# Kernel tuning notes

Hardware: AMD Instinct MI355X
Metric: run time of the kernel (lower is better)

## Reference

```python
import jax, jax.numpy as jnp
from jax import lax
import numpy as np

CHUNK = 64


def short_conv(x, w):
    # depthwise causal conv1d: x (B,L,D), w (D,K)
    L = x.shape[1]
    K = w.shape[1]
    xp = jnp.pad(x, ((0, 0), (K - 1, 0), (0, 0)))
    return sum(xp[:, j:j + L, :] * w[:, j] for j in range(K))


def o2b_weighted_delta_rule(k, q, v, b):
    # k,q,v,b: (B,L,H,D) float32, zero initial state
    B, L, H, D = k.shape
    C = CHUNK
    Nc = L // C

    def to_chunks(t):  # (B,L,H,D) -> (Nc,B,H,C,D)
        return t.transpose(0, 2, 1, 3).reshape(B, H, Nc, C, D).transpose(2, 0, 1, 3, 4)

    Kc, Qc, Vc, Bc = map(to_chunks, (k, q, v, b))
    eyeC = jnp.eye(C, dtype=jnp.float32)
    W0 = jnp.zeros((B, H, D, D), jnp.float32)
    Cf = float(C)

    def step(carry, xs):
        W_t, W_avg = carry
        i, Ki, Qi, Vi, Bi = xs
        KiT = jnp.swapaxes(Ki, -1, -2)
        T = jnp.tril(Bi @ KiT, k=-1)                      # (B,H,C,C) strictly lower
        inv = jnp.linalg.inv(eyeC + T)
        Ui = inv @ (Vi - Bi @ W_t)                        # (B,H,C,D)
        W_new = W_t + KiT @ Ui
        ts = (i * C).astype(jnp.float32)                  # init t == 0 for all batches
        idx = jnp.arange(1, C + 1, dtype=jnp.float32) + ts  # (C,)
        cs = jnp.cumsum(idx)
        weighted_idx = idx + idx.sum() - cs
        w_i = (weighted_idx / ((1 + ts + Cf) * (ts + Cf) / 2))[:, None]  # (C,1)
        coef1 = ts / (ts + Cf) * ((1 + ts) / (1 + ts + Cf))
        coef2 = Cf / (ts + Cf) * ((ts * 2 + 1 + Cf) / (1 + ts + Cf))
        W_avg_new = coef1 * W_avg + coef2 * W_t + KiT @ (Ui * w_i)
        tri0 = (1 + ts) * ts / 2
        a = (tri0 / (tri0 + cs))[:, None]                 # (C,1)
        c = 1.0 - a
        r = cs[:, None]                                   # (C,1)
        j_idx = (cs - idx)[None, :]                       # (1,C)
        T_mat = jnp.where(r >= j_idx, (r - j_idx) / (tri0 + r), 0.0)  # (C,C)
        O_i = (Qi @ W_avg) * a + (Qi @ W_t) * c + (T_mat * (Qi @ KiT)) @ Ui
        return (W_new, W_avg_new), O_i

    (_, _), O = lax.scan(step, (W0, W0), (jnp.arange(Nc), Kc, Qc, Vc, Bc))
    # O: (Nc,B,H,C,D) -> (B,L,H,D)
    return O.transpose(1, 2, 0, 3, 4).reshape(B, H, L, D).transpose(0, 2, 1, 3)


def setup_inputs() -> dict:
    key = jax.random.key(0)
    ks = jax.random.split(key, 9)
    B, L, Dm, H = 4, 2048, 1024, 16
    Dh, K = Dm // H, 4
    s = 0.02
    return {
        'x': jax.random.normal(ks[0], (B, L, Dm), jnp.float32),
        'Wk': s * jax.random.normal(ks[1], (Dm, Dm), jnp.float32),
        'bk': jnp.zeros((Dm,), jnp.float32),
        'Wq': s * jax.random.normal(ks[2], (Dm, Dm), jnp.float32),
        'bq': jnp.zeros((Dm,), jnp.float32),
        'Wv': s * jax.random.normal(ks[3], (Dm, Dm), jnp.float32),
        'bv': jnp.zeros((Dm,), jnp.float32),
        'Wbeta': s * jax.random.normal(ks[4], (H, Dm), jnp.float32),
        'bbeta': jnp.zeros((H,), jnp.float32),
        'conv_k': 0.1 * jax.random.normal(ks[5], (Dm, K), jnp.float32),
        'conv_q': 0.1 * jax.random.normal(ks[6], (Dm, K), jnp.float32),
        'conv_v': 0.1 * jax.random.normal(ks[7], (Dm, K), jnp.float32),
        'rms_w': jnp.ones((Dh,), jnp.float32),
        'Wout': s * jax.random.normal(ks[8], (Dm, Dm), jnp.float32),
        'bout': jnp.zeros((Dm,), jnp.float32),
    }


def reference(x, Wk, bk, Wq, bq, Wv, bv, Wbeta, bbeta, conv_k, conv_q, conv_v, rms_w, Wout, bout):
    B, L, Dm = x.shape
    H = Wbeta.shape[0]
    Dh = Dm // H
    k = short_conv(x @ Wk.T + bk, conv_k)
    q = short_conv(x @ Wq.T + bq, conv_q)
    v = short_conv(x @ Wv.T + bv, conv_v)
    beta = jax.nn.sigmoid(x @ Wbeta.T + bbeta)            # (B,L,H)
    k = k.reshape(B, L, H, Dh)
    q = q.reshape(B, L, H, Dh)
    v = jax.nn.silu(v.reshape(B, L, H, Dh))
    knorm = jnp.linalg.norm(k, axis=-1, keepdims=True)
    qnorm = jnp.linalg.norm(q, axis=-1, keepdims=True)
    k = k / (knorm + 1e-6)
    q = q / (qnorm + 1e-6)
    eta = beta  # eta coefficient = 1.0, ogd_mode='deltanet'
    b = eta[..., None] * k
    v = eta[..., None] * v
    o = o2b_weighted_delta_rule(k, q, v, b)               # (B,L,H,Dh)
    o = o * jax.lax.rsqrt(jnp.mean(o * o, axis=-1, keepdims=True) + 1e-6) * rms_w
    o = o.reshape(B, L, Dm)
    return o @ Wout.T + bout
```

## Files before the change

### kernel.cpp

```cpp
#include <hip/hip_runtime.h>

typedef __attribute__((ext_vector_type(8))) short bf16x8;
typedef __attribute__((ext_vector_type(4))) float f32x4;

#define MFMA(a, b, c) __builtin_amdgcn_mfma_f32_16x16x32_bf16((a), (b), (c), 0, 0, 0)

__device__ inline unsigned short f2bf_rne(float f) {
  unsigned int u = __float_as_uint(f);
  u += 0x7FFFu + ((u >> 16) & 1u);
  return (unsigned short)(u >> 16);
}

__global__ __launch_bounds__(256) void cast_bf16_kernel(const float* __restrict__ in,
                                                        unsigned short* __restrict__ out,
                                                        int n4) {
  const int i = blockIdx.x * 256 + threadIdx.x;
  if (i >= n4) return;
  const float4 v = ((const float4*)in)[i];
  ushort4 o;
  o.x = f2bf_rne(v.x); o.y = f2bf_rne(v.y); o.z = f2bf_rne(v.z); o.w = f2bf_rne(v.w);
  ((ushort4*)out)[i] = o;
}

__global__ __launch_bounds__(256) void concat_bias_kernel(const float* __restrict__ bk,
                                                          const float* __restrict__ bq,
                                                          const float* __restrict__ bv,
                                                          float* __restrict__ b3) {
  const int i = blockIdx.x * 256 + threadIdx.x;
  if (i < 1024) b3[i] = bk[i];
  else if (i < 2048) b3[i] = bq[i - 1024];
  else if (i < 3072) b3[i] = bv[i - 2048];
}

__global__ __launch_bounds__(256) void gemm_bf16_nt(
    const unsigned short* __restrict__ A, const unsigned short* __restrict__ Bw,
    const float* __restrict__ bias, float* __restrict__ C, int M, int N, int K) {
  __shared__ unsigned short Asl[128 * 32];
  __shared__ unsigned short Bsl[128 * 32];
  const int tid = threadIdx.x;
  const int lane = tid & 63, w = tid >> 6;
  const int bm = blockIdx.x * 128, bn = blockIdx.y * 128;
  const int wr = (w >> 1) * 64, wc = (w & 1) * 64;

  const int li0 = tid, li1 = tid + 256;
  const int ar0 = li0 >> 2, ak0 = (li0 & 3) * 8;
  const int ar1 = li1 >> 2, ak1 = (li1 & 3) * 8;
  const unsigned short* gA0 = A + (size_t)(bm + ar0) * K + ak0;
  const unsigned short* gA1 = A + (size_t)(bm + ar1) * K + ak1;
  const unsigned short* gB0 = Bw + (size_t)(bn + ar0) * K + ak0;
  const unsigned short* gB1 = Bw + (size_t)(bn + ar1) * K + ak1;
  unsigned short* lA0 = &Asl[(size_t)(w * 64) * 8];
  unsigned short* lA1 = &Asl[(size_t)(w * 64 + 256) * 8];
  unsigned short* lB0 = &Bsl[(size_t)(w * 64) * 8];
  unsigned short* lB1 = &Bsl[(size_t)(w * 64 + 256) * 8];

  f32x4 acc[4][4];
#pragma unroll
  for (int i = 0; i < 4; ++i)
#pragma unroll
    for (int j = 0; j < 4; ++j) acc[i][j] = (f32x4){0.f, 0.f, 0.f, 0.f};

  const int fr = lane & 15, kg = lane >> 4;

  for (int k0 = 0; k0 < K; k0 += 32) {
    __syncthreads();
    __builtin_amdgcn_global_load_lds((const __attribute__((address_space(1))) unsigned int*)(gA0 + k0),
                                     (__attribute__((address_space(3))) unsigned int*)lA0, 16, 0, 0);
    __builtin_amdgcn_global_load_lds((const __attribute__((address_space(1))) unsigned int*)(gA1 + k0),
                                     (__attribute__((address_space(3))) unsigned int*)lA1, 16, 0, 0);
    __builtin_amdgcn_global_load_lds((const __attribute__((address_space(1))) unsigned int*)(gB0 + k0),
                                     (__attribute__((address_space(3))) unsigned int*)lB0, 16, 0, 0);
    __builtin_amdgcn_global_load_lds((const __attribute__((address_space(1))) unsigned int*)(gB1 + k0),
                                     (__attribute__((address_space(3))) unsigned int*)lB1, 16, 0, 0);
    __syncthreads();

    bf16x8 af[4], bfr[4];
#pragma unroll
    for (int i = 0; i < 4; ++i) {
      af[i] = *(const bf16x8*)&Asl[(size_t)(wr + i * 16 + fr) * 32 + kg * 8];
      bfr[i] = *(const bf16x8*)&Bsl[(size_t)(wc + i * 16 + fr) * 32 + kg * 8];
    }
#pragma unroll
    for (int i = 0; i < 4; ++i)
#pragma unroll
      for (int j = 0; j < 4; ++j)
        acc[i][j] = MFMA(af[i], bfr[j], acc[i][j]);
  }

  const int og = lane >> 4;
#pragma unroll
  for (int j = 0; j < 4; ++j) {
    const int col = bn + wc + j * 16 + fr;
    const float bs = bias[col];
#pragma unroll
    for (int i = 0; i < 4; ++i) {
#pragma unroll
      for (int r = 0; r < 4; ++r) {
        const int row = bm + wr + i * 16 + og * 4 + r;
        C[(size_t)row * N + col] = acc[i][j][r] + bs;
      }
    }
  }
}

__global__ __launch_bounds__(256) void beta_kernel(const float* __restrict__ x,
                                                   const float* __restrict__ Wb,
                                                   const float* __restrict__ bb,
                                                   float* __restrict__ beta) {
  const int m = blockIdx.x;
  const int tid = threadIdx.x;
  const int h = tid >> 4;
  const int l = tid & 15;
  const float4* x4 = (const float4*)(x + (size_t)m * 1024);
  const float4* w4 = (const float4*)(Wb + (size_t)h * 1024);
  float acc = 0.f;
#pragma unroll 4
  for (int jj = 0; jj < 16; ++jj) {
    float4 xv = x4[l + 16 * jj];
    float4 wv = w4[l + 16 * jj];
    acc += xv.x * wv.x + xv.y * wv.y + xv.z * wv.z + xv.w * wv.w;
  }
  acc += __shfl_xor(acc, 1);
  acc += __shfl_xor(acc, 2);
  acc += __shfl_xor(acc, 4);
  acc += __shfl_xor(acc, 8);
  if (l == 0) {
    const float s = acc + bb[h];
    beta[(size_t)m * 16 + h] = 1.f / (1.f + expf(-s));
  }
}

__global__ __launch_bounds__(256) void prep_kernel(
    const float* __restrict__ qkv, const float* __restrict__ betab,
    const float* __restrict__ convk, const float* __restrict__ convq,
    const float* __restrict__ convv,
    unsigned short* __restrict__ kn16, unsigned short* __restrict__ qn16,
    float* __restrict__ vz) {
  const int m = blockIdx.x;
  const int l = m & 2047;
  const int lane = threadIdx.x & 63;
  const int wvi = threadIdx.x >> 6;
#pragma unroll
  for (int s = 0; s < 4; ++s) {
    const int h = 4 * s + wvi;
    const int c = h * 64 + lane;
    const float4 wk4 = *(const float4*)(convk + (size_t)c * 4);
    const float4 wq4 = *(const float4*)(convq + (size_t)c * 4);
    const float4 wv4 = *(const float4*)(convv + (size_t)c * 4);
    const float wk[4] = {wk4.x, wk4.y, wk4.z, wk4.w};
    const float wq[4] = {wq4.x, wq4.y, wq4.z, wq4.w};
    const float wvv[4] = {wv4.x, wv4.y, wv4.z, wv4.w};
    float kc = 0.f, qc = 0.f, vc = 0.f;
#pragma unroll
    for (int j = 0; j < 4; ++j) {
      const int lj = l - 3 + j;
      if (lj >= 0) {
        const size_t rb = (size_t)(m - l + lj) * 3072 + c;
        kc += wk[j] * qkv[rb];
        qc += wq[j] * qkv[rb + 1024];
        vc += wvv[j] * qkv[rb + 2048];
      }
    }
    float ssk = kc * kc, ssq = qc * qc;
    ssk += __shfl_xor(ssk, 1); ssq += __shfl_xor(ssq, 1);
    ssk += __shfl_xor(ssk, 2); ssq += __shfl_xor(ssq, 2);
    ssk += __shfl_xor(ssk, 4); ssq += __shfl_xor(ssq, 4);
    ssk += __shfl_xor(ssk, 8); ssq += __shfl_xor(ssq, 8);
    ssk += __shfl_xor(ssk, 16); ssq += __shfl_xor(ssq, 16);
    ssk += __shfl_xor(ssk, 32); ssq += __shfl_xor(ssq, 32);
    const float eta = betab[(size_t)m * 16 + h];
    const size_t o = (size_t)m * 1024 + c;
    kn16[o] = f2bf_rne(kc / (sqrtf(ssk) + 1e-6f));
    qn16[o] = f2bf_rne(qc / (sqrtf(ssq) + 1e-6f));
    vz[o] = eta * vc / (1.f + expf(-vc));
  }
}

#define LDB 72
#define LDV 68

__global__ __launch_bounds__(512, 1) void scan_kernel(
    const unsigned short* __restrict__ kn16, const unsigned short* __restrict__ qn16,
    const float* __restrict__ vz, const float* __restrict__ betab,
    float* __restrict__ O) {
  __shared__ unsigned short Kb[64 * LDB], Qb[64 * LDB], Ktb[64 * LDB];
  __shared__ unsigned short Wtb[64 * LDB], Wavgtb[64 * LDB];
  __shared__ unsigned short Pb[2][64 * LDB], Ptb[2][64 * LDB], Ztb[2][64 * LDB];
  __shared__ unsigned short P1b[64 * LDB], Utwb[64 * LDB];
  __shared__ float Vs[64 * LDV];
  __shared__ float etas[64];

  const int tid = threadIdx.x;
  const int bh = blockIdx.x;
  const int b = bh >> 4, h = bh & 15;
  const int wv = tid >> 6, lane = tid & 63;
  const int fr = lane & 15, og = lane >> 4;
  const int i0 = (wv >> 2) * 2, i1 = i0 + 1, j = wv & 3;
  const int gcol = j * 16 + fr;
  const int row0 = i0 * 16 + og * 4;
  const int row1 = i1 * 16 + og * 4;

  for (int t = tid; t < 64 * LDB; t += 512) { Wtb[t] = 0; Wavgtb[t] = 0; }

  const size_t base = ((size_t)b * 2048) * 1024 + (size_t)h * 64;
  const unsigned short* kp = kn16 + base;
  const unsigned short* qp = qn16 + base;
  const float* vp = vz + base;
  const float* etap = betab + (size_t)b * 2048 * 16 + h;
  float* Op = O + (size_t)bh * 2048 * 64;

  f32x4 Wt[2], Wav[2];
  Wt[0] = Wt[1] = Wav[0] = Wav[1] = (f32x4){0.f, 0.f, 0.f, 0.f};

  const int sr = tid >> 3, sc8 = (tid & 7) * 8;
  __syncthreads();

#pragma unroll 1
  for (int ic = 0; ic < 32; ++ic) {
    const float ts = (float)(ic * 64);

    {
      const size_t g = (size_t)(ic * 64 + sr) * 1024 + sc8;
      *(ushort4*)&Kb[sr * LDB + sc8] = *(const ushort4*)(kp + g);
      *(ushort4*)&Kb[sr * LDB + sc8 + 4] = *(const ushort4*)(kp + g + 4);
      *(ushort4*)&Qb[sr * LDB + sc8] = *(const ushort4*)(qp + g);
      *(ushort4*)&Qb[sr * LDB + sc8 + 4] = *(const ushort4*)(qp + g + 4);
      *(float4*)&Vs[sr * LDV + sc8] = *(const float4*)(vp + g);
      *(float4*)&Vs[sr * LDV + sc8 + 4] = *(const float4*)(vp + g + 4);
      unsigned short tv[8];
#pragma unroll
      for (int i = 0; i < 8; ++i)
        tv[i] = kp[(size_t)(ic * 64 + sc8 + i) * 1024 + sr];
      ushort4 t0v = {tv[0], tv[1], tv[2], tv[3]}, t1v = {tv[4], tv[5], tv[6], tv[7]};
      *(ushort4*)&Ktb[sr * LDB + sc8] = t0v;
      *(ushort4*)&Ktb[sr * LDB + sc8 + 4] = t1v;
      if (tid < 64) etas[tid] = etap[(size_t)(ic * 64 + tid) * 16];
    }
    __syncthreads();

    f32x4 Zacc[2], RHSs[2];
    {
      bf16x8 aK0[2], aK1[2], bK[2], bW[2];
#pragma unroll
      for (int t = 0; t < 2; ++t) {
        aK0[t] = *(const bf16x8*)&Kb[(i0 * 16 + fr) * LDB + t * 32 + og * 8];
        aK1[t] = *(const bf16x8*)&Kb[(i1 * 16 + fr) * LDB + t * 32 + og * 8];
        bK[t] = *(const bf16x8*)&Kb[(j * 16 + fr) * LDB + t * 32 + og * 8];
        bW[t] = *(const bf16x8*)&Wtb[(j * 16 + fr) * LDB + t * 32 + og * 8];
      }
      f32x4 accT0 = {0, 0, 0, 0}, accT1 = {0, 0, 0, 0};
      f32x4 accR0 = {0, 0, 0, 0}, accR1 = {0, 0, 0, 0};
#pragma unroll
      for (int t = 0; t < 2; ++t) {
        accT0 = MFMA(aK0[t], bK[t], accT0);
        accT1 = MFMA(aK1[t], bK[t], accT1);
        accR0 = MFMA(aK0[t], bW[t], accR0);
        accR1 = MFMA(aK1[t], bW[t], accR1);
      }
#pragma unroll
      for (int s = 0; s < 2; ++s) {
        const int rb = s ? row1 : row0;
        const f32x4 aT = s ? accT1 : accT0;
        const f32x4 aR = s ? accR1 : accR0;
        unsigned short us[4];
        float zv[4];
#pragma unroll
        for (int r = 0; r < 4; ++r) {
          const int grow = rb + r;
          const float eta = etas[grow];
          const float tvv = (gcol < grow) ? -eta * aT[r] : 0.f;
          us[r] = f2bf_rne(tvv);
          zv[r] = Vs[grow * LDV + gcol] - eta * aR[r];
          Pb[0][grow * LDB + gcol] = us[r];
          P1b[grow * LDB + gcol] = us[r];
        }
        ushort4 pp = {us[0], us[1], us[2], us[3]};
        *(ushort4*)&Ptb[0][gcol * LDB + rb] = pp;
        ushort4 zp = {f2bf_rne(zv[0]), f2bf_rne(zv[1]), f2bf_rne(zv[2]), f2bf_rne(zv[3])};
        *(ushort4*)&Ztb[0][gcol * LDB + rb] = zp;
        Zacc[s] = (f32x4){zv[0], zv[1], zv[2], zv[3]};
        RHSs[s] = Zacc[s];
      }
    }
    __syncthreads();

#pragma unroll
    for (int k = 0; k < 6; ++k) {
      const int cur = k & 1, nxt = cur ^ 1;
      bf16x8 aP0[2], aP1[2], bZ[2];
#pragma unroll
      for (int t = 0; t < 2; ++t) {
        aP0[t] = *(const bf16x8*)&Pb[cur][(i0 * 16 + fr) * LDB + t * 32 + og * 8];
        aP1[t] = *(const bf16x8*)&Pb[cur][(i1 * 16 + fr) * LDB + t * 32 + og * 8];
        bZ[t] = *(const bf16x8*)&Ztb[cur][(j * 16 + fr) * LDB + t * 32 + og * 8];
      }
      f32x4 sq0 = {0, 0, 0, 0}, sq1 = {0, 0, 0, 0};
      if (k < 5) {
#pragma unroll
        for (int t = 0; t < 2; ++t) {
          bf16x8 bPt = *(const bf16x8*)&Ptb[cur][(j * 16 + fr) * LDB + t * 32 + og * 8];
          sq0 = MFMA(aP0[t], bPt, sq0);
          sq1 = MFMA(aP1[t], bPt, sq1);
        }
      }
#pragma unroll
      for (int t = 0; t < 2; ++t) {
        Zacc[0] = MFMA(aP0[t], bZ[t], Zacc[0]);
        Zacc[1] = MFMA(aP1[t], bZ[t], Zacc[1]);
      }
#pragma unroll
      for (int s = 0; s < 2; ++s) {
        const int rb = s ? row1 : row0;
        const f32x4 zz = Zacc[s];
        ushort4 zp = {f2bf_rne(zz[0]), f2bf_rne(zz[1]), f2bf_rne(zz[2]), f2bf_rne(zz[3])};
        *(ushort4*)&Ztb[nxt][gcol * LDB + rb] = zp;
        if (k < 5) {
          const f32x4 sv = s ? sq1 : sq0;
          unsigned short u0 = f2bf_rne(sv[0]), u1 = f2bf_rne(sv[1]);
          unsigned short u2 = f2bf_rne(sv[2]), u3 = f2bf_rne(sv[3]);
          Pb[nxt][(rb + 0) * LDB + gcol] = u0;
          Pb[nxt][(rb + 1) * LDB + gcol] = u1;
          Pb[nxt][(rb + 2) * LDB + gcol] = u2;
          Pb[nxt][(rb + 3) * LDB + gcol] = u3;
          ushort4 pp = {u0, u1, u2, u3};
          *(ushort4*)&Ptb[nxt][gcol * LDB + rb] = pp;
        }
      }
      __syncthreads();
    }

    bf16x8 a0[2], a1[2];
    {
#pragma unroll
      for (int t = 0; t < 2; ++t) {
        a0[t] = *(const bf16x8*)&P1b[(i0 * 16 + fr) * LDB + t * 32 + og * 8];
        a1[t] = *(const bf16x8*)&P1b[(i1 * 16 + fr) * LDB + t * 32 + og * 8];
      }
      f32x4 R0 = RHSs[0] - Zacc[0];
      f32x4 R1 = RHSs[1] - Zacc[1];
#pragma unroll
      for (int t = 0; t < 2; ++t) {
        bf16x8 bU = *(const bf16x8*)&Ztb[0][(j * 16 + fr) * LDB + t * 32 + og * 8];
        R0 = MFMA(a0[t], bU, R0);
        R1 = MFMA(a1[t], bU, R1);
      }
      ushort4 r0p = {f2bf_rne(R0[0]), f2bf_rne(R0[1]), f2bf_rne(R0[2]), f2bf_rne(R0[3])};
      ushort4 r1p = {f2bf_rne(R1[0]), f2bf_rne(R1[1]), f2bf_rne(R1[2]), f2bf_rne(R1[3])};
      *(ushort4*)&Pb[1][gcol * LDB + row0] = r0p;
      *(ushort4*)&Pb[1][gcol * LDB + row1] = r1p;
      RHSs[0] = R0;
      RHSs[1] = R1;
    }
    __syncthreads();

    {
      f32x4 dU0 = RHSs[0], dU1 = RHSs[1];
#pragma unroll
      for (int t = 0; t < 2; ++t) {
        bf16x8 bR = *(const bf16x8*)&Pb[1][(j * 16 + fr) * LDB + t * 32 + og * 8];
        dU0 = MFMA(a0[t], bR, dU0);
        dU1 = MFMA(a1[t], bR, dU1);
      }
      Zacc[0] += dU0;
      Zacc[1] += dU1;
      const float invden = 1.f / (0.5f * (ts + 65.f) * (ts + 64.f));
#pragma unroll
      for (int s = 0; s < 2; ++s) {
        const int rb = s ? row1 : row0;
        const f32x4 uu = Zacc[s];
        ushort4 up = {f2bf_rne(uu[0]), f2bf_rne(uu[1]), f2bf_rne(uu[2]), f2bf_rne(uu[3])};
        *(ushort4*)&Ztb[0][gcol * LDB + rb] = up;
        unsigned short uw[4];
#pragma unroll
        for (int r = 0; r < 4; ++r) {
          const float rr = (float)(rb + r);
          const float wr = (ts * (64.f - rr) + (rr + 1.f) + 2080.f -
                            0.5f * (rr + 1.f) * (rr + 2.f)) * invden;
          uw[r] = f2bf_rne(uu[r] * wr);
        }
        ushort4 uwp = {uw[0], uw[1], uw[2], uw[3]};
        *(ushort4*)&Utwb[gcol * LDB + rb] = uwp;
      }
    }
    f32x4 Oacc[2];
    {
      bf16x8 aQ0[2], aQ1[2], bKj[2], bWt2[2], bWa2[2];
#pragma unroll
      for (int t = 0; t < 2; ++t) {
        aQ0[t] = *(const bf16x8*)&Qb[(i0 * 16 + fr) * LDB + t * 32 + og * 8];
        aQ1[t] = *(const bf16x8*)&Qb[(i1 * 16 + fr) * LDB + t * 32 + og * 8];
        bKj[t] = *(const bf16x8*)&Kb[(j * 16 + fr) * LDB + t * 32 + og * 8];
        bWt2[t] = *(const bf16x8*)&Wtb[(j * 16 + fr) * LDB + t * 32 + og * 8];
        bWa2[t] = *(const bf16x8*)&Wavgtb[(j * 16 + fr) * LDB + t * 32 + og * 8];
      }
      f32x4 aS0 = {0, 0, 0, 0}, aS1 = {0, 0, 0, 0};
      f32x4 aA0 = {0, 0, 0, 0}, aA1 = {0, 0, 0, 0};
      f32x4 aC0 = {0, 0, 0, 0}, aC1 = {0, 0, 0, 0};
#pragma unroll
      for (int t = 0; t < 2; ++t) {
        aS0 = MFMA(aQ0[t], bKj[t], aS0);
        aS1 = MFMA(aQ1[t], bKj[t], aS1);
        aA0 = MFMA(aQ0[t], bWa2[t], aA0);
        aA1 = MFMA(aQ1[t], bWa2[t], aA1);
        aC0 = MFMA(aQ0[t], bWt2[t], aC0);
        aC1 = MFMA(aQ1[t], bWt2[t], aC1);
      }
      const float tri0 = 0.5f * ts * (ts + 1.f);
      const float jidx = gcol * ts + 0.5f * gcol * (gcol + 1.f);
#pragma unroll
      for (int s = 0; s < 2; ++s) {
        const int rb = s ? row1 : row0;
        const f32x4 sS = s ? aS1 : aS0;
        const f32x4 sA = s ? aA1 : aA0;
        const f32x4 sC = s ? aC1 : aC0;
        f32x4 oo;
#pragma unroll
        for (int r = 0; r < 4; ++r) {
          const float grow = (float)(rb + r);
          const float csr = (grow + 1.f) * ts + 0.5f * (grow + 1.f) * (grow + 2.f);
          const float rinv = 1.f / (tri0 + csr);
          const float av = tri0 * rinv;
          oo[r] = av * sA[r] + (1.f - av) * sC[r];
          const float svv = (csr >= jidx) ? (csr - jidx) * rinv * sS[r] : 0.f;
          Ptb[1][(rb + r) * LDB + gcol] = f2bf_rne(svv);
        }
        Oacc[s] = oo;
      }
    }
    __syncthreads();

    {
      bf16x8 aS0[2], aS1[2], bU2[2];
#pragma unroll
      for (int t = 0; t < 2; ++t) {
        aS0[t] = *(const bf16x8*)&Ptb[1][(i0 * 16 + fr) * LDB + t * 32 + og * 8];
        aS1[t] = *(const bf16x8*)&Ptb[1][(i1 * 16 + fr) * LDB + t * 32 + og * 8];
        bU2[t] = *(const bf16x8*)&Ztb[0][(j * 16 + fr) * LDB + t * 32 + og * 8];
      }
#pragma unroll
      for (int t = 0; t < 2; ++t) {
        Oacc[0] = MFMA(aS0[t], bU2[t], Oacc[0]);
        Oacc[1] = MFMA(aS1[t], bU2[t], Oacc[1]);
      }
#pragma unroll
      for (int s = 0; s < 2; ++s) {
        const int rb = s ? row1 : row0;
#pragma unroll
        for (int r = 0; r < 4; ++r)
          Op[(size_t)(ic * 64 + rb + r) * 64 + gcol] = Oacc[s][r];
      }
    }

    {
      bf16x8 aU0[2], aU1[2], aW0[2], aW1[2], bKt2[2];
#pragma unroll
      for (int t = 0; t < 2; ++t) {
        aU0[t] = *(const bf16x8*)&Ztb[0][(i0 * 16 + fr) * LDB + t * 32 + og * 8];
        aU1[t] = *(const bf16x8*)&Ztb[0][(i1 * 16 + fr) * LDB + t * 32 + og * 8];
        aW0[t] = *(const bf16x8*)&Utwb[(i0 * 16 + fr) * LDB + t * 32 + og * 8];
        aW1[t] = *(const bf16x8*)&Utwb[(i1 * 16 + fr) * LDB + t * 32 + og * 8];
        bKt2[t] = *(const bf16x8*)&Ktb[(j * 16 + fr) * LDB + t * 32 + og * 8];
      }
      const float den = (ts + 64.f) * (ts + 65.f);
      const float cc1 = ts * (ts + 1.f) / den;
      const float cc2 = 64.f * (2.f * ts + 65.f) / den;
      f32x4 wn0 = cc1 * Wav[0] + cc2 * Wt[0];
      f32x4 wn1 = cc1 * Wav[1] + cc2 * Wt[1];
#pragma unroll
      for (int t = 0; t < 2; ++t) {
        wn0 = MFMA(aW0[t], bKt2[t], wn0);
        wn1 = MFMA(aW1[t], bKt2[t], wn1);
        Wt[0] = MFMA(aU0[t], bKt2[t], Wt[0]);
        Wt[1] = MFMA(aU1[t], bKt2[t], Wt[1]);
      }
      Wav[0] = wn0;
      Wav[1] = wn1;
#pragma unroll
      for (int s = 0; s < 2; ++s) {
        const int rb = s ? row1 : row0;
        const f32x4 wtv = Wt[s];
        const f32x4 wav2 = Wav[s];
#pragma unroll
        for (int r = 0; r < 4; ++r) {
          Wtb[(rb + r) * LDB + gcol] = f2bf_rne(wtv[r]);
          Wavgtb[(rb + r) * LDB + gcol] = f2bf_rne(wav2[r]);
        }
      }
    }
    __syncthreads();
  }
}

__global__ __launch_bounds__(256) void rms_kernel(const float* __restrict__ O,
                                                  const float* __restrict__ rmsw,
                                                  unsigned short* __restrict__ out16) {
  const int m = blockIdx.x;
  const int b = m >> 11, l = m & 2047;
  const int wv = threadIdx.x >> 6, lane = threadIdx.x & 63;
  const float rw = rmsw[lane];
#pragma unroll
  for (int hh = 0; hh < 4; ++hh) {
    const int h = wv * 4 + hh;
    const float v = O[(((size_t)(b * 16 + h)) * 2048 + l) * 64 + lane];
    float ss = v * v;
    ss += __shfl_xor(ss, 1); ss += __shfl_xor(ss, 2); ss += __shfl_xor(ss, 4);
    ss += __shfl_xor(ss, 8); ss += __shfl_xor(ss, 16); ss += __shfl_xor(ss, 32);
    const float sc = rsqrtf(ss * (1.f / 64.f) + 1e-6f);
    out16[(size_t)m * 1024 + h * 64 + lane] = f2bf_rne(v * sc * rw);
  }
}

extern "C" void kernel_launch(void* const* d_in, const int* in_sizes, int n_in,
                              void* d_out, int out_size, void* d_ws, size_t ws_size,
                              hipStream_t stream) {
  (void)in_sizes; (void)n_in; (void)out_size; (void)ws_size;
  const float* x     = (const float*)d_in[0];
  const float* Wk    = (const float*)d_in[1];
  const float* bk    = (const float*)d_in[2];
  const float* Wq    = (const float*)d_in[3];
  const float* bq    = (const float*)d_in[4];
  const float* Wv    = (const float*)d_in[5];
  const float* bv    = (const float*)d_in[6];
  const float* Wbeta = (const float*)d_in[7];
  const float* bbeta = (const float*)d_in[8];
  const float* convk = (const float*)d_in[9];
  const float* convq = (const float*)d_in[10];
  const float* convv = (const float*)d_in[11];
  const float* rmsw  = (const float*)d_in[12];
  const float* Wout  = (const float*)d_in[13];
  const float* bout  = (const float*)d_in[14];
  float* out = (float*)d_out;
  float* ws = (float*)d_ws;

  const size_t SZ = (size_t)8192 * 1024;
  float* qkv = ws;
  float* betab = ws + 3 * SZ;
  unsigned short* x16 = (unsigned short*)(ws + 3 * SZ + 131072);
  unsigned short* wk16 = x16 + SZ;
  unsigned short* wq16 = wk16 + 1048576;
  unsigned short* wv16 = wq16 + 1048576;
  unsigned short* wo16 = wv16 + 1048576;
  unsigned short* kn16 = wo16 + 1048576;
  unsigned short* qn16 = kn16 + SZ;
  float* b3 = (float*)(qn16 + SZ);
  float* vzb = out;
  float* Obuf = qkv;
  unsigned short* normed16 = (unsigned short*)(ws + SZ);

  dim3 blk(256);
  hipLaunchKernelGGL(cast_bf16_kernel, dim3(8192), blk, 0, stream, x, x16, (int)(SZ / 4));
  hipLaunchKernelGGL(cast_bf16_kernel, dim3(1024), blk, 0, stream, Wk, wk16, 262144);
  hipLaunchKernelGGL(cast_bf16_kernel, dim3(1024), blk, 0, stream, Wq, wq16, 262144);
  hipLaunchKernelGGL(cast_bf16_kernel, dim3(1024), blk, 0, stream, Wv, wv16, 262144);
  hipLaunchKernelGGL(cast_bf16_kernel, dim3(1024), blk, 0, stream, Wout, wo16, 262144);
  hipLaunchKernelGGL(concat_bias_kernel, dim3(12), blk, 0, stream, bk, bq, bv, b3);

  hipLaunchKernelGGL(gemm_bf16_nt, dim3(64, 24), blk, 0, stream, x16, wk16, b3,
                     qkv, 8192, 3072, 1024);
  hipLaunchKernelGGL(beta_kernel, dim3(8192), blk, 0, stream, x, Wbeta, bbeta, betab);
  hipLaunchKernelGGL(prep_kernel, dim3(8192), blk, 0, stream, qkv, betab,
                     convk, convq, convv, kn16, qn16, vzb);
  hipLaunchKernelGGL(scan_kernel, dim3(64), dim3(512), 0, stream, kn16, qn16, vzb,
                     betab, Obuf);
  hipLaunchKernelGGL(rms_kernel, dim3(8192), blk, 0, stream, Obuf, rmsw, normed16);
  hipLaunchKernelGGL(gemm_bf16_nt, dim3(64, 8), blk, 0, stream, normed16, wo16, bout, out,
                     8192, 1024, 1024);
}
```

Measured before the change: 586.1 us.

## Prefetch next chunk in scan, fuse cast and beta kernels into fewer launches

The scan kernel now double-buffers K and Q in shared memory and prefetches the next chunk's K, Q, transposed K, V and eta into registers while the current chunk computes. This removes the per-chunk load phase and its barrier from the serial critical path. Separately, the five cast kernels and the bias concat are merged into one grid-stride kernel, and the beta projection plus sigmoid is folded into prep_kernel, cutting launches and a global round trip. The cost is higher register and shared-memory use in the scan kernel, plus redundant final-chunk loads.

```diff
diff --git a/kernel.cpp b/kernel.cpp
--- a/kernel.cpp
+++ b/kernel.cpp
@@ -11,25 +11,37 @@
   return (unsigned short)(u >> 16);
 }
 
-__global__ __launch_bounds__(256) void cast_bf16_kernel(const float* __restrict__ in,
-                                                        unsigned short* __restrict__ out,
-                                                        int n4) {
-  const int i = blockIdx.x * 256 + threadIdx.x;
-  if (i >= n4) return;
-  const float4 v = ((const float4*)in)[i];
-  ushort4 o;
-  o.x = f2bf_rne(v.x); o.y = f2bf_rne(v.y); o.z = f2bf_rne(v.z); o.w = f2bf_rne(v.w);
-  ((ushort4*)out)[i] = o;
-}
-
-__global__ __launch_bounds__(256) void concat_bias_kernel(const float* __restrict__ bk,
-                                                          const float* __restrict__ bq,
-                                                          const float* __restrict__ bv,
-                                                          float* __restrict__ b3) {
-  const int i = blockIdx.x * 256 + threadIdx.x;
-  if (i < 1024) b3[i] = bk[i];
-  else if (i < 2048) b3[i] = bq[i - 1024];
-  else if (i < 3072) b3[i] = bv[i - 2048];
+__global__ __launch_bounds__(256) void prepare_kernel(
+    const float* __restrict__ x, const float* __restrict__ Wk,
+    const float* __restrict__ Wq, const float* __restrict__ Wv,
+    const float* __restrict__ Wout, const float* __restrict__ bk,
+    const float* __restrict__ bq, const float* __restrict__ bv,
+    unsigned short* __restrict__ x16, unsigned short* __restrict__ wk16,
+    unsigned short* __restrict__ wq16, unsigned short* __restrict__ wv16,
+    unsigned short* __restrict__ wo16, float* __restrict__ b3) {
+  const int gid = blockIdx.x * 256 + threadIdx.x;
+  const int stride = gridDim.x * 256;
+  for (int i = gid; i < 2097152; i += stride) {
+    const float4 v = ((const float4*)x)[i];
+    ushort4 o = {f2bf_rne(v.x), f2bf_rne(v.y), f2bf_rne(v.z), f2bf_rne(v.w)};
+    ((ushort4*)x16)[i] = o;
+  }
+  for (int i = gid; i < 262144; i += stride) {
+    float4 v = ((const float4*)Wk)[i];
+    ushort4 o = {f2bf_rne(v.x), f2bf_rne(v.y), f2bf_rne(v.z), f2bf_rne(v.w)};
+    ((ushort4*)wk16)[i] = o;
+    v = ((const float4*)Wq)[i];
+    o = (ushort4){f2bf_rne(v.x), f2bf_rne(v.y), f2bf_rne(v.z), f2bf_rne(v.w)};
+    ((ushort4*)wq16)[i] = o;
+    v = ((const float4*)Wv)[i];
+    o = (ushort4){f2bf_rne(v.x), f2bf_rne(v.y), f2bf_rne(v.z), f2bf_rne(v.w)};
+    ((ushort4*)wv16)[i] = o;
+    v = ((const float4*)Wout)[i];
+    o = (ushort4){f2bf_rne(v.x), f2bf_rne(v.y), f2bf_rne(v.z), f2bf_rne(v.w)};
+    ((ushort4*)wo16)[i] = o;
+  }
+  if (gid < 3072)
+    b3[gid] = gid < 1024 ? bk[gid] : gid < 2048 ? bq[gid - 1024] : bv[gid - 2048];
 }
 
 __global__ __launch_bounds__(256) void gemm_bf16_nt(
@@ -103,43 +115,45 @@
   }
 }
 
-__global__ __launch_bounds__(256) void beta_kernel(const float* __restrict__ x,
-                                                   const float* __restrict__ Wb,
-                                                   const float* __restrict__ bb,
-                                                   float* __restrict__ beta) {
-  const int m = blockIdx.x;
-  const int tid = threadIdx.x;
-  const int h = tid >> 4;
-  const int l = tid & 15;
-  const float4* x4 = (const float4*)(x + (size_t)m * 1024);
-  const float4* w4 = (const float4*)(Wb + (size_t)h * 1024);
-  float acc = 0.f;
-#pragma unroll 4
-  for (int jj = 0; jj < 16; ++jj) {
-    float4 xv = x4[l + 16 * jj];
-    float4 wv = w4[l + 16 * jj];
-    acc += xv.x * wv.x + xv.y * wv.y + xv.z * wv.z + xv.w * wv.w;
-  }
-  acc += __shfl_xor(acc, 1);
-  acc += __shfl_xor(acc, 2);
-  acc += __shfl_xor(acc, 4);
-  acc += __shfl_xor(acc, 8);
-  if (l == 0) {
-    const float s = acc + bb[h];
-    beta[(size_t)m * 16 + h] = 1.f / (1.f + expf(-s));
-  }
-}
-
 __global__ __launch_bounds__(256) void prep_kernel(
-    const float* __restrict__ qkv, const float* __restrict__ betab,
+    const float* __restrict__ x, const float* __restrict__ qkv,
+    const float* __restrict__ Wbeta, const float* __restrict__ bbeta,
     const float* __restrict__ convk, const float* __restrict__ convq,
-    const float* __restrict__ convv,
+    const float* __restrict__ convv, float* __restrict__ betab,
     unsigned short* __restrict__ kn16, unsigned short* __restrict__ qn16,
     float* __restrict__ vz) {
+  __shared__ float etas_sm[16];
   const int m = blockIdx.x;
   const int l = m & 2047;
   const int lane = threadIdx.x & 63;
   const int wvi = threadIdx.x >> 6;
+
+  {
+    const float4* xr = (const float4*)(x + (size_t)m * 1024);
+    const float4 xv0 = xr[lane], xv1 = xr[lane + 64];
+    const float4 xv2 = xr[lane + 128], xv3 = xr[lane + 192];
+#pragma unroll
+    for (int hh = 0; hh < 4; ++hh) {
+      const int h = wvi * 4 + hh;
+      const float4* wr = (const float4*)(Wbeta + (size_t)h * 1024);
+      const float4 w0 = wr[lane], w1 = wr[lane + 64];
+      const float4 w2 = wr[lane + 128], w3 = wr[lane + 192];
+      float acc = xv0.x * w0.x + xv0.y * w0.y + xv0.z * w0.z + xv0.w * w0.w +
+                  xv1.x * w1.x + xv1.y * w1.y + xv1.z * w1.z + xv1.w * w1.w +
+                  xv2.x * w2.x + xv2.y * w2.y + xv2.z * w2.z + xv2.w * w2.w +
+                  xv3.x * w3.x + xv3.y * w3.y + xv3.z * w3.z + xv3.w * w3.w;
+      acc += __shfl_xor(acc, 1); acc += __shfl_xor(acc, 2);
+      acc += __shfl_xor(acc, 4); acc += __shfl_xor(acc, 8);
+      acc += __shfl_xor(acc, 16); acc += __shfl_xor(acc, 32);
+      if (lane == 0) {
+        const float e = 1.f / (1.f + expf(-(acc + bbeta[h])));
+        etas_sm[h] = e;
+        betab[(size_t)m * 16 + h] = e;
+      }
+    }
+  }
+  __syncthreads();
+
 #pragma unroll
   for (int s = 0; s < 4; ++s) {
     const int h = 4 * s + wvi;
@@ -152,13 +166,13 @@
     const float wvv[4] = {wv4.x, wv4.y, wv4.z, wv4.w};
     float kc = 0.f, qc = 0.f, vc = 0.f;
 #pragma unroll
-    for (int j = 0; j < 4; ++j) {
-      const int lj = l - 3 + j;
+    for (int jj = 0; jj < 4; ++jj) {
+      const int lj = l - 3 + jj;
       if (lj >= 0) {
         const size_t rb = (size_t)(m - l + lj) * 3072 + c;
-        kc += wk[j] * qkv[rb];
-        qc += wq[j] * qkv[rb + 1024];
-        vc += wvv[j] * qkv[rb + 2048];
+        kc += wk[jj] * qkv[rb];
+        qc += wq[jj] * qkv[rb + 1024];
+        vc += wvv[jj] * qkv[rb + 2048];
       }
     }
     float ssk = kc * kc, ssq = qc * qc;
@@ -168,7 +182,7 @@
     ssk += __shfl_xor(ssk, 8); ssq += __shfl_xor(ssq, 8);
     ssk += __shfl_xor(ssk, 16); ssq += __shfl_xor(ssq, 16);
     ssk += __shfl_xor(ssk, 32); ssq += __shfl_xor(ssq, 32);
-    const float eta = betab[(size_t)m * 16 + h];
+    const float eta = etas_sm[h];
     const size_t o = (size_t)m * 1024 + c;
     kn16[o] = f2bf_rne(kc / (sqrtf(ssk) + 1e-6f));
     qn16[o] = f2bf_rne(qc / (sqrtf(ssq) + 1e-6f));
@@ -177,18 +191,15 @@
 }
 
 #define LDB 72
-#define LDV 68
 
 __global__ __launch_bounds__(512, 1) void scan_kernel(
     const unsigned short* __restrict__ kn16, const unsigned short* __restrict__ qn16,
     const float* __restrict__ vz, const float* __restrict__ betab,
     float* __restrict__ O) {
-  __shared__ unsigned short Kb[64 * LDB], Qb[64 * LDB], Ktb[64 * LDB];
+  __shared__ unsigned short Kb[2][64 * LDB], Qb[2][64 * LDB], Ktb[64 * LDB];
   __shared__ unsigned short Wtb[64 * LDB], Wavgtb[64 * LDB];
   __shared__ unsigned short Pb[2][64 * LDB], Ptb[2][64 * LDB], Ztb[2][64 * LDB];
   __shared__ unsigned short P1b[64 * LDB], Utwb[64 * LDB];
-  __shared__ float Vs[64 * LDV];
-  __shared__ float etas[64];
 
   const int tid = threadIdx.x;
   const int bh = blockIdx.x;
@@ -213,39 +224,66 @@
   Wt[0] = Wt[1] = Wav[0] = Wav[1] = (f32x4){0.f, 0.f, 0.f, 0.f};
 
   const int sr = tid >> 3, sc8 = (tid & 7) * 8;
+
+  {
+    const size_t g = (size_t)sr * 1024 + sc8;
+    *(ushort4*)&Kb[0][sr * LDB + sc8] = *(const ushort4*)(kp + g);
+    *(ushort4*)&Kb[0][sr * LDB + sc8 + 4] = *(const ushort4*)(kp + g + 4);
+    *(ushort4*)&Qb[0][sr * LDB + sc8] = *(const ushort4*)(qp + g);
+    *(ushort4*)&Qb[0][sr * LDB + sc8 + 4] = *(const ushort4*)(qp + g + 4);
+    ushort4 t0v, t1v;
+    t0v.x = kp[(size_t)(sc8 + 0) * 1024 + sr];
+    t0v.y = kp[(size_t)(sc8 + 1) * 1024 + sr];
+    t0v.z = kp[(size_t)(sc8 + 2) * 1024 + sr];
+    t0v.w = kp[(size_t)(sc8 + 3) * 1024 + sr];
+    t1v.x = kp[(size_t)(sc8 + 4) * 1024 + sr];
+    t1v.y = kp[(size_t)(sc8 + 5) * 1024 + sr];
+    t1v.z = kp[(size_t)(sc8 + 6) * 1024 + sr];
+    t1v.w = kp[(size_t)(sc8 + 7) * 1024 + sr];
+    *(ushort4*)&Ktb[sr * LDB + sc8] = t0v;
+    *(ushort4*)&Ktb[sr * LDB + sc8 + 4] = t1v;
+  }
+  float vr0[4], vr1[4], er0[4], er1[4];
+#pragma unroll
+  for (int r = 0; r < 4; ++r) {
+    vr0[r] = vp[(size_t)(row0 + r) * 1024 + gcol];
+    vr1[r] = vp[(size_t)(row1 + r) * 1024 + gcol];
+    er0[r] = etap[(size_t)(row0 + r) * 16];
+    er1[r] = etap[(size_t)(row1 + r) * 16];
+  }
+  ushort4 pk0, pk1, pq0, pq1, pt0, pt1;
   __syncthreads();
 
 #pragma unroll 1
   for (int ic = 0; ic < 32; ++ic) {
+    const int cur = ic & 1, nxt = cur ^ 1;
     const float ts = (float)(ic * 64);
-
-    {
-      const size_t g = (size_t)(ic * 64 + sr) * 1024 + sc8;
-      *(ushort4*)&Kb[sr * LDB + sc8] = *(const ushort4*)(kp + g);
-      *(ushort4*)&Kb[sr * LDB + sc8 + 4] = *(const ushort4*)(kp + g + 4);
-      *(ushort4*)&Qb[sr * LDB + sc8] = *(const ushort4*)(qp + g);
-      *(ushort4*)&Qb[sr * LDB + sc8 + 4] = *(const ushort4*)(qp + g + 4);
-      *(float4*)&Vs[sr * LDV + sc8] = *(const float4*)(vp + g);
-      *(float4*)&Vs[sr * LDV + sc8 + 4] = *(const float4*)(vp + g + 4);
-      unsigned short tv[8];
-#pragma unroll
-      for (int i = 0; i < 8; ++i)
-        tv[i] = kp[(size_t)(ic * 64 + sc8 + i) * 1024 + sr];
-      ushort4 t0v = {tv[0], tv[1], tv[2], tv[3]}, t1v = {tv[4], tv[5], tv[6], tv[7]};
-      *(ushort4*)&Ktb[sr * LDB + sc8] = t0v;
-      *(ushort4*)&Ktb[sr * LDB + sc8 + 4] = t1v;
-      if (tid < 64) etas[tid] = etap[(size_t)(ic * 64 + tid) * 16];
-    }
-    __syncthreads();
+    const int icn = (ic < 31) ? ic + 1 : ic;
 
     f32x4 Zacc[2], RHSs[2];
     {
+      if (ic > 0) {
+        *(ushort4*)&Ktb[sr * LDB + sc8] = pt0;
+        *(ushort4*)&Ktb[sr * LDB + sc8 + 4] = pt1;
+      }
+      const size_t gn = (size_t)(icn * 64 + sr) * 1024 + sc8;
+      pk0 = *(const ushort4*)(kp + gn);
+      pk1 = *(const ushort4*)(kp + gn + 4);
+      pq0 = *(const ushort4*)(qp + gn);
+      pq1 = *(const ushort4*)(qp + gn + 4);
+      {
+        const size_t cb = (size_t)(icn * 64 + sc8);
+        pt0.x = kp[(cb + 0) * 1024 + sr]; pt0.y = kp[(cb + 1) * 1024 + sr];
+        pt0.z = kp[(cb + 2) * 1024 + sr]; pt0.w = kp[(cb + 3) * 1024 + sr];
+        pt1.x = kp[(cb + 4) * 1024 + sr]; pt1.y = kp[(cb + 5) * 1024 + sr];
+        pt1.z = kp[(cb + 6) * 1024 + sr]; pt1.w = kp[(cb + 7) * 1024 + sr];
+      }
       bf16x8 aK0[2], aK1[2], bK[2], bW[2];
 #pragma unroll
       for (int t = 0; t < 2; ++t) {
-        aK0[t] = *(const bf16x8*)&Kb[(i0 * 16 + fr) * LDB + t * 32 + og * 8];
-        aK1[t] = *(const bf16x8*)&Kb[(i1 * 16 + fr) * LDB + t * 32 + og * 8];
-        bK[t] = *(const bf16x8*)&Kb[(j * 16 + fr) * LDB + t * 32 + og * 8];
+        aK0[t] = *(const bf16x8*)&Kb[cur][(i0 * 16 + fr) * LDB + t * 32 + og * 8];
+        aK1[t] = *(const bf16x8*)&Kb[cur][(i1 * 16 + fr) * LDB + t * 32 + og * 8];
+        bK[t] = *(const bf16x8*)&Kb[cur][(j * 16 + fr) * LDB + t * 32 + og * 8];
         bW[t] = *(const bf16x8*)&Wtb[(j * 16 + fr) * LDB + t * 32 + og * 8];
       }
       f32x4 accT0 = {0, 0, 0, 0}, accT1 = {0, 0, 0, 0};
@@ -267,10 +305,11 @@
 #pragma unroll
         for (int r = 0; r < 4; ++r) {
           const int grow = rb + r;
-          const float eta = etas[grow];
+          const float eta = s ? er1[r] : er0[r];
+          const float vv = s ? vr1[r] : vr0[r];
           const float tvv = (gcol < grow) ? -eta * aT[r] : 0.f;
           us[r] = f2bf_rne(tvv);
-          zv[r] = Vs[grow * LDV + gcol] - eta * aR[r];
+          zv[r] = vv - eta * aR[r];
           Pb[0][grow * LDB + gcol] = us[r];
           P1b[grow * LDB + gcol] = us[r];
         }
@@ -286,19 +325,19 @@
 
 #pragma unroll
     for (int k = 0; k < 6; ++k) {
-      const int cur = k & 1, nxt = cur ^ 1;
+      const int pc = k & 1, pn = pc ^ 1;
       bf16x8 aP0[2], aP1[2], bZ[2];
 #pragma unroll
       for (int t = 0; t < 2; ++t) {
-        aP0[t] = *(const bf16x8*)&Pb[cur][(i0 * 16 + fr) * LDB + t * 32 + og * 8];
-        aP1[t] = *(const bf16x8*)&Pb[cur][(i1 * 16 + fr) * LDB + t * 32 + og * 8];
-        bZ[t] = *(const bf16x8*)&Ztb[cur][(j * 16 + fr) * LDB + t * 32 + og * 8];
+        aP0[t] = *(const bf16x8*)&Pb[pc][(i0 * 16 + fr) * LDB + t * 32 + og * 8];
+        aP1[t] = *(const bf16x8*)&Pb[pc][(i1 * 16 + fr) * LDB + t * 32 + og * 8];
+        bZ[t] = *(const bf16x8*)&Ztb[pc][(j * 16 + fr) * LDB + t * 32 + og * 8];
       }
       f32x4 sq0 = {0, 0, 0, 0}, sq1 = {0, 0, 0, 0};
       if (k < 5) {
 #pragma unroll
         for (int t = 0; t < 2; ++t) {
-          bf16x8 bPt = *(const bf16x8*)&Ptb[cur][(j * 16 + fr) * LDB + t * 32 + og * 8];
+          bf16x8 bPt = *(const bf16x8*)&Ptb[pc][(j * 16 + fr) * LDB + t * 32 + og * 8];
           sq0 = MFMA(aP0[t], bPt, sq0);
           sq1 = MFMA(aP1[t], bPt, sq1);
         }
@@ -313,17 +352,17 @@
         const int rb = s ? row1 : row0;
         const f32x4 zz = Zacc[s];
         ushort4 zp = {f2bf_rne(zz[0]), f2bf_rne(zz[1]), f2bf_rne(zz[2]), f2bf_rne(zz[3])};
-        *(ushort4*)&Ztb[nxt][gcol * LDB + rb] = zp;
+        *(ushort4*)&Ztb[pn][gcol * LDB + rb] = zp;
         if (k < 5) {
           const f32x4 sv = s ? sq1 : sq0;
           unsigned short u0 = f2bf_rne(sv[0]), u1 = f2bf_rne(sv[1]);
           unsigned short u2 = f2bf_rne(sv[2]), u3 = f2bf_rne(sv[3]);
-          Pb[nxt][(rb + 0) * LDB + gcol] = u0;
-          Pb[nxt][(rb + 1) * LDB + gcol] = u1;
-          Pb[nxt][(rb + 2) * LDB + gcol] = u2;
-          Pb[nxt][(rb + 3) * LDB + gcol] = u3;
+          Pb[pn][(rb + 0) * LDB + gcol] = u0;
+          Pb[pn][(rb + 1) * LDB + gcol] = u1;
+          Pb[pn][(rb + 2) * LDB + gcol] = u2;
+          Pb[pn][(rb + 3) * LDB + gcol] = u3;
           ushort4 pp = {u0, u1, u2, u3};
-          *(ushort4*)&Ptb[nxt][gcol * LDB + rb] = pp;
+          *(ushort4*)&Ptb[pn][gcol * LDB + rb] = pp;
         }
       }
       __syncthreads();
@@ -331,6 +370,10 @@
 
     bf16x8 a0[2], a1[2];
     {
+      *(ushort4*)&Kb[nxt][sr * LDB + sc8] = pk0;
+      *(ushort4*)&Kb[nxt][sr * LDB + sc8 + 4] = pk1;
+      *(ushort4*)&Qb[nxt][sr * LDB + sc8] = pq0;
+      *(ushort4*)&Qb[nxt][sr * LDB + sc8 + 4] = pq1;
 #pragma unroll
       for (int t = 0; t < 2; ++t) {
         a0[t] = *(const bf16x8*)&P1b[(i0 * 16 + fr) * LDB + t * 32 + og * 8];
@@ -363,6 +406,13 @@
       }
       Zacc[0] += dU0;
       Zacc[1] += dU1;
+#pragma unroll
+      for (int r = 0; r < 4; ++r) {
+        vr0[r] = vp[(size_t)(icn * 64 + row0 + r) * 1024 + gcol];
+        vr1[r] = vp[(size_t)(icn * 64 + row1 + r) * 1024 + gcol];
+        er0[r] = etap[(size_t)(icn * 64 + row0 + r) * 16];
+        er1[r] = etap[(size_t)(icn * 64 + row1 + r) * 16];
+      }
       const float invden = 1.f / (0.5f * (ts + 65.f) * (ts + 64.f));
 #pragma unroll
       for (int s = 0; s < 2; ++s) {
@@ -387,9 +437,9 @@
       bf16x8 aQ0[2], aQ1[2], bKj[2], bWt2[2], bWa2[2];
 #pragma unroll
       for (int t = 0; t < 2; ++t) {
-        aQ0[t] = *(const bf16x8*)&Qb[(i0 * 16 + fr) * LDB + t * 32 + og * 8];
-        aQ1[t] = *(const bf16x8*)&Qb[(i1 * 16 + fr) * LDB + t * 32 + og * 8];
-        bKj[t] = *(const bf16x8*)&Kb[(j * 16 + fr) * LDB + t * 32 + og * 8];
+        aQ0[t] = *(const bf16x8*)&Qb[cur][(i0 * 16 + fr) * LDB + t * 32 + og * 8];
+        aQ1[t] = *(const bf16x8*)&Qb[cur][(i1 * 16 + fr) * LDB + t * 32 + og * 8];
+        bKj[t] = *(const bf16x8*)&Kb[cur][(j * 16 + fr) * LDB + t * 32 + og * 8];
         bWt2[t] = *(const bf16x8*)&Wtb[(j * 16 + fr) * LDB + t * 32 + og * 8];
         bWa2[t] = *(const bf16x8*)&Wavgtb[(j * 16 + fr) * LDB + t * 32 + og * 8];
       }
@@ -548,18 +598,12 @@
   unsigned short* normed16 = (unsigned short*)(ws + SZ);
 
   dim3 blk(256);
-  hipLaunchKernelGGL(cast_bf16_kernel, dim3(8192), blk, 0, stream, x, x16, (int)(SZ / 4));
-  hipLaunchKernelGGL(cast_bf16_kernel, dim3(1024), blk, 0, stream, Wk, wk16, 262144);
-  hipLaunchKernelGGL(cast_bf16_kernel, dim3(1024), blk, 0, stream, Wq, wq16, 262144);
-  hipLaunchKernelGGL(cast_bf16_kernel, dim3(1024), blk, 0, stream, Wv, wv16, 262144);
-  hipLaunchKernelGGL(cast_bf16_kernel, dim3(1024), blk, 0, stream, Wout, wo16, 262144);
-  hipLaunchKernelGGL(concat_bias_kernel, dim3(12), blk, 0, stream, bk, bq, bv, b3);
-
+  hipLaunchKernelGGL(prepare_kernel, dim3(2048), blk, 0, stream, x, Wk, Wq, Wv, Wout,
+                     bk, bq, bv, x16, wk16, wq16, wv16, wo16, b3);
   hipLaunchKernelGGL(gemm_bf16_nt, dim3(64, 24), blk, 0, stream, x16, wk16, b3,
                      qkv, 8192, 3072, 1024);
-  hipLaunchKernelGGL(beta_kernel, dim3(8192), blk, 0, stream, x, Wbeta, bbeta, betab);
-  hipLaunchKernelGGL(prep_kernel, dim3(8192), blk, 0, stream, qkv, betab,
-                     convk, convq, convv, kn16, qn16, vzb);
+  hipLaunchKernelGGL(prep_kernel, dim3(8192), blk, 0, stream, x, qkv, Wbeta, bbeta,
+                     convk, convq, convv, betab, kn16, qn16, vzb);
   hipLaunchKernelGGL(scan_kernel, dim3(64), dim3(512), 0, stream, kn16, qn16, vzb,
                      betab, Obuf);
   hipLaunchKernelGGL(rms_kernel, dim3(8192), blk, 0, stream, Obuf, rmsw, normed16);
```

Result: faster. 546.0 us (-6.8%).
